# Kernel tuning notes

Measured on AMD Instinct MI355X. Metric: run time of the kernel, lower is better.

The kernel has to match this reference:

```python
import jax, jax.numpy as jnp
import numpy as np

EPS = 1e-5  # torch LayerNorm default
N_BLOCKS = 8
N_NODES = 4096
BATCH = 4096


def setup_inputs() -> dict:
    key = jax.random.key(0)
    ks = jax.random.split(key, 4)
    scale = 1.0 / np.sqrt(N_NODES)  # keep activations sane through 8 GEMMs
    x = jax.random.normal(ks[0], (BATCH, N_NODES), dtype=jnp.float32)
    W = jax.random.normal(ks[1], (N_BLOCKS, N_NODES, N_NODES), dtype=jnp.float32) * scale
    b = jax.random.normal(ks[2], (N_BLOCKS, N_NODES), dtype=jnp.float32) * 0.01
    slope = jax.random.uniform(ks[3], (N_BLOCKS, N_NODES), dtype=jnp.float32)
    ln_g = jnp.ones((N_BLOCKS, N_NODES), dtype=jnp.float32)
    ln_b = jnp.zeros((N_BLOCKS, N_NODES), dtype=jnp.float32)
    return {"x": x, "ln_g": ln_g, "ln_b": ln_b, "W": W, "b": b, "slope": slope}


def _block(x, g, bt, Wi, bi, si):
    # LayerNorm over last dim (biased variance, eps inside sqrt) -> Linear -> per-feature LeakyReLU
    mu = jnp.mean(x, axis=-1, keepdims=True)
    var = jnp.mean(jnp.square(x - mu), axis=-1, keepdims=True)
    ln = (x - mu) * jax.lax.rsqrt(var + EPS) * g + bt
    y = jnp.einsum('bn,mn->bm', ln, Wi) + bi  # torch Linear: x @ W.T + b
    return jnp.where(y < 0, y * si, y)


def reference(x, ln_g, ln_b, W, b, slope):
    for i in range(N_BLOCKS):
        x = _block(x, ln_g[i], ln_b[i], W[i], b[i], slope[i])
    return x
```

## Files before the change

### kernel.cpp

```cpp
#include <hip/hip_runtime.h>
#include <hip/hip_bf16.h>

#define NNODES 4096
#define NBATCH 4096
#define NBLK 8
#define LN_EPS 1e-5f

typedef __attribute__((ext_vector_type(8))) short short8;
typedef __attribute__((ext_vector_type(4))) float f32x4;
typedef __attribute__((ext_vector_type(4))) unsigned short u16x4;
typedef unsigned short u16;

__device__ __forceinline__ u16 bf16_rn(float f) {
  unsigned int u = __builtin_bit_cast(unsigned int, f);
  u += 0x7fffu + ((u >> 16) & 1u);
  return (u16)(u >> 16);
}

__device__ __forceinline__ float bf16_to_f(u16 h) {
  unsigned int u = ((unsigned int)h) << 16;
  return __builtin_bit_cast(float, u);
}

__device__ __forceinline__ void load_lds16(const void* g, void* l) {
  __builtin_amdgcn_global_load_lds((const __attribute__((address_space(1))) void*)g,
                                   (__attribute__((address_space(3))) void*)l,
                                   16, 0, 0);
}

template <bool LNF32>
__global__ __launch_bounds__(256) void prep_kernel(const float* __restrict__ W,
                                                   u16* __restrict__ Wb,
                                                   const void* __restrict__ xin,
                                                   const float* __restrict__ g,
                                                   const float* __restrict__ bt,
                                                   u16* __restrict__ lnout) {
  __shared__ float sh[8];
  int t = threadIdx.x;
  if (blockIdx.x < 16384) {
    int idx = blockIdx.x * 256 + t;
    float4 v = ((const float4*)W)[idx];
    u16x4 o;
    o[0] = bf16_rn(v.x); o[1] = bf16_rn(v.y); o[2] = bf16_rn(v.z); o[3] = bf16_rn(v.w);
    ((u16x4*)Wb)[idx] = o;
    return;
  }
  int row = blockIdx.x - 16384;
  float f[16];
  float s = 0.f, ss = 0.f;
  const float4* xr = (const float4*)((const float*)xin + (size_t)row * NNODES);
#pragma unroll
  for (int q = 0; q < 4; ++q) {
    float4 v = xr[q * 256 + t];
    f[q * 4 + 0] = v.x; f[q * 4 + 1] = v.y; f[q * 4 + 2] = v.z; f[q * 4 + 3] = v.w;
    s  += v.x + v.y + v.z + v.w;
    ss += v.x * v.x + v.y * v.y + v.z * v.z + v.w * v.w;
  }
#pragma unroll
  for (int off = 32; off >= 1; off >>= 1) {
    s  += __shfl_xor(s, off, 64);
    ss += __shfl_xor(ss, off, 64);
  }
  int wid = t >> 6, lane = t & 63;
  if (lane == 0) { sh[wid] = s; sh[wid + 4] = ss; }
  __syncthreads();
  s  = sh[0] + sh[1] + sh[2] + sh[3];
  ss = sh[4] + sh[5] + sh[6] + sh[7];
  float mu  = s * (1.f / NNODES);
  float var = ss * (1.f / NNODES) - mu * mu;
  float rs  = rsqrtf(var + LN_EPS);
  u16x4* o = (u16x4*)(lnout + (size_t)row * NNODES);
  const float4* gv = (const float4*)g;
  const float4* bv = (const float4*)bt;
#pragma unroll
  for (int q = 0; q < 4; ++q) {
    int i = q * 256 + t;
    float4 gg = gv[i], bb = bv[i];
    u16x4 ov;
    ov[0] = bf16_rn((f[q * 4 + 0] - mu) * rs * gg.x + bb.x);
    ov[1] = bf16_rn((f[q * 4 + 1] - mu) * rs * gg.y + bb.y);
    ov[2] = bf16_rn((f[q * 4 + 2] - mu) * rs * gg.z + bb.z);
    ov[3] = bf16_rn((f[q * 4 + 3] - mu) * rs * gg.w + bb.w);
    o[i] = ov;
  }
}

__global__ __launch_bounds__(256) void ln_bf16_kernel(const u16* __restrict__ x,
                                                      const float* __restrict__ g,
                                                      const float* __restrict__ bt,
                                                      u16* __restrict__ out) {
  int row = blockIdx.x;
  int t = threadIdx.x;
  const u16* xr = x + (size_t)row * NNODES;
  float f[2][8];
  float s = 0.f, ss = 0.f;
#pragma unroll
  for (int q = 0; q < 2; ++q) {
    short8 v = *(const short8*)(xr + q * 2048 + t * 8);
#pragma unroll
    for (int j = 0; j < 8; ++j) {
      float fv = bf16_to_f((u16)v[j]);
      f[q][j] = fv;
      s += fv; ss += fv * fv;
    }
  }
#pragma unroll
  for (int off = 32; off >= 1; off >>= 1) {
    s  += __shfl_xor(s, off, 64);
    ss += __shfl_xor(ss, off, 64);
  }
  __shared__ float sh[8];
  int wid = t >> 6, lane = t & 63;
  if (lane == 0) { sh[wid] = s; sh[wid + 4] = ss; }
  __syncthreads();
  s  = sh[0] + sh[1] + sh[2] + sh[3];
  ss = sh[4] + sh[5] + sh[6] + sh[7];
  float mu  = s * (1.f / NNODES);
  float var = ss * (1.f / NNODES) - mu * mu;
  float rs  = rsqrtf(var + LN_EPS);
  const float4* gv = (const float4*)g;
  const float4* bv = (const float4*)bt;
#pragma unroll
  for (int q = 0; q < 2; ++q) {
    int base = q * 2048 + t * 8;
    float4 g0 = gv[base / 4], g1 = gv[base / 4 + 1];
    float4 b0 = bv[base / 4], b1 = bv[base / 4 + 1];
    short8 sv;
    sv[0] = (short)bf16_rn((f[q][0] - mu) * rs * g0.x + b0.x);
    sv[1] = (short)bf16_rn((f[q][1] - mu) * rs * g0.y + b0.y);
    sv[2] = (short)bf16_rn((f[q][2] - mu) * rs * g0.z + b0.z);
    sv[3] = (short)bf16_rn((f[q][3] - mu) * rs * g0.w + b0.w);
    sv[4] = (short)bf16_rn((f[q][4] - mu) * rs * g1.x + b1.x);
    sv[5] = (short)bf16_rn((f[q][5] - mu) * rs * g1.y + b1.y);
    sv[6] = (short)bf16_rn((f[q][6] - mu) * rs * g1.z + b1.z);
    sv[7] = (short)bf16_rn((f[q][7] - mu) * rs * g1.w + b1.w);
    *(short8*)(out + (size_t)row * NNODES + base) = sv;
  }
}


#define VMC(N) asm volatile("s_waitcnt vmcnt(" #N ")" ::: "memory")

#define STAGE_A(T, H)                                                          \
  { load_lds16(Asrc0 + (size_t)((H) * 128) * Kdim + (T) * 64,                  \
               ldsA + ((T) & 1) * 16384 + (H) * 8192 + tid * 8);               \
    load_lds16(Asrc0 + (size_t)((H) * 128 + 64) * Kdim + (T) * 64,             \
               ldsA + ((T) & 1) * 16384 + (H) * 8192 + 4096 + tid * 8); }

#define STAGE_B(T, H)                                                          \
  { load_lds16(Bsrc0 + (size_t)((H) * 128) * Kdim + (T) * 64,                  \
               ldsB + ((T) & 1) * 16384 + (H) * 8192 + tid * 8);               \
    load_lds16(Bsrc0 + (size_t)((H) * 128 + 64) * Kdim + (T) * 64,             \
               ldsB + ((T) & 1) * 16384 + (H) * 8192 + 4096 + tid * 8); }

#define CVSTORE(SRC, CIDX)                                                     \
  { __builtin_amdgcn_sched_barrier(0);                                         \
    u16x4 o_;                                                                  \
    o_[0] = bf16_rn(SRC[0]); o_[1] = bf16_rn(SRC[1]);                          \
    o_[2] = bf16_rn(SRC[2]); o_[3] = bf16_rn(SRC[3]);                          \
    *(u16x4*)(Wnd + cvoff + (size_t)(CIDX) * 2048) = o_; }

#define CONVP3                                                                 \
  { if (CONVON && t < 16) {                                                    \
      const float* cp_ = Wns + cvoff + (size_t)(2 * t) * 2048;                 \
      asm volatile("global_load_dwordx4 %0, %1, off"                           \
                   : "=&v"(cvA) : "v"(cp_) : "memory");                        \
    }                                                                          \
    VMC(4);                                                                    \
    if (CONVON && t >= 1 && t <= 16) CVSTORE(cvB, 2 * t - 1) }

#define CONVP7                                                                 \
  { if (CONVON && t < 16) {                                                    \
      const float* cp_ = Wns + cvoff + (size_t)(2 * t + 1) * 2048;             \
      asm volatile("global_load_dwordx4 %0, %1, off"                           \
                   : "=&v"(cvB) : "v"(cp_) : "memory");                        \
    }                                                                          \
    VMC(4);                                                                    \
    if (CONVON && t < 16) CVSTORE(cvA, 2 * t) }

#define PH(KT, MH, NH, STAGE_STMT, VM_STMT)                                    \
  {                                                                            \
    const u16* Ab = ldsA + ((KT) & 1) * 16384 + aBase + (MH) * 4096;           \
    const u16* Bb = ldsB + ((KT) & 1) * 16384 + bBase + (NH) * 2048;           \
    if ((NH) == 0) {                                                           \
      _Pragma("unroll") for (int mi = 0; mi < 4; ++mi) {                       \
        afr[mi][0] = *(const short8*)(Ab + mi * 1024 + gk0);                   \
        afr[mi][1] = *(const short8*)(Ab + mi * 1024 + gk1);                   \
      }                                                                        \
    }                                                                          \
    if ((MH) == 0) {                                                           \
      _Pragma("unroll") for (int ni = 0; ni < 2; ++ni) {                       \
        bfr[NH][ni][0] = *(const short8*)(Bb + ni * 1024 + gk0);               \
        bfr[NH][ni][1] = *(const short8*)(Bb + ni * 1024 + gk1);               \
      }                                                                        \
    }                                                                          \
    STAGE_STMT;                                                                \
    if ((NH) == 0 && (MH) == 0)                                                \
      asm volatile("s_waitcnt lgkmcnt(8)" ::: "memory");                       \
    VM_STMT;                                                                   \
    __builtin_amdgcn_s_barrier();                                              \
    asm volatile("s_waitcnt lgkmcnt(0)" ::: "memory");                         \
    __builtin_amdgcn_sched_barrier(0);                                         \
    __builtin_amdgcn_s_setprio(1);                                             \
    _Pragma("unroll") for (int mi = 0; mi < 4; ++mi)                           \
      _Pragma("unroll") for (int ni = 0; ni < 2; ++ni) {                       \
        acc[(MH) * 4 + mi][(NH) * 2 + ni] =                                    \
          __builtin_amdgcn_mfma_f32_16x16x32_bf16(afr[mi][0], bfr[NH][ni][0],  \
            acc[(MH) * 4 + mi][(NH) * 2 + ni], 0, 0, 0);                       \
        acc[(MH) * 4 + mi][(NH) * 2 + ni] =                                    \
          __builtin_amdgcn_mfma_f32_16x16x32_bf16(afr[mi][1], bfr[NH][ni][1],  \
            acc[(MH) * 4 + mi][(NH) * 2 + ni], 0, 0, 0);                       \
      }                                                                        \
    __builtin_amdgcn_s_setprio(0);                                             \
    __builtin_amdgcn_s_barrier();                                              \
  }

template <bool OUTF32, bool CONVON>
__global__ __launch_bounds__(512, 2) void gemm256_kernel(const u16* __restrict__ A,
                                                         const u16* __restrict__ B,
                                                         const float* __restrict__ bias,
                                                         const float* __restrict__ slope,
                                                         void* __restrict__ Cv,
                                                         const float* __restrict__ Wns,
                                                         u16* __restrict__ Wnd) {
  constexpr int Kdim = NNODES;
  __shared__ u16 lds[65536];
  u16* ldsA = lds;
  u16* ldsB = lds + 32768;

  const int tid  = threadIdx.x;
  const int lane = tid & 63;
  const int wid  = tid >> 6;
  const int wr   = wid >> 2;
  const int wc   = wid & 3;

  int bid = blockIdx.x;
  int swz = (bid & 7) * 32 + (bid >> 3);
  const int brow = (swz >> 4) * 256;
  const int bcol = (swz & 15) * 256;

  const int srow = tid >> 3;
  const int sg   = ((tid & 7) ^ (srow & 7)) * 8;
  const u16* Asrc0 = A + (size_t)(brow + srow) * Kdim + sg;
  const u16* Bsrc0 = B + (size_t)(bcol + srow) * Kdim + sg;

  const int r16 = lane & 15, kq = lane >> 4;
  const int g0  = kq ^ (r16 & 7);
  const int gk0 = g0 * 8, gk1 = (g0 ^ 4) * 8;
  const int aBase = wr * 8192 + r16 * 64;
  const int bBase = (wc >> 1) * 8192 + ((wc & 1) * 64 + r16) * 64;

  const size_t cvoff = (size_t)bid * 65536 + tid * 4;
  f32x4 cvA, cvB;

  f32x4 acc[8][4] = {};
  short8 afr[4][2], bfr[2][2][2];

  STAGE_B(0, 0) STAGE_B(0, 1) STAGE_A(0, 0) STAGE_A(0, 1) STAGE_B(1, 0) STAGE_B(1, 1)
  VMC(4);
  __builtin_amdgcn_s_barrier();

  for (int t = 0; t < 31; ++t) {
    const int T = 2 * t;
    PH(T,     0, 0, STAGE_A(T + 1, 0), ;)
    PH(T,     0, 1, STAGE_A(T + 1, 1), ;)
    PH(T,     1, 0, STAGE_B(T + 2, 0), ;)
    PH(T,     1, 1, STAGE_B(T + 2, 1), CONVP3)
    PH(T + 1, 0, 0, STAGE_A(T + 2, 0), ;)
    PH(T + 1, 0, 1, STAGE_A(T + 2, 1), ;)
    PH(T + 1, 1, 0, STAGE_B(T + 3, 0), ;)
    PH(T + 1, 1, 1, STAGE_B(T + 3, 1), CONVP7)
  }
  PH(62, 0, 0, STAGE_A(63, 0), ;)
  PH(62, 0, 1, STAGE_A(63, 1), ;)
  PH(62, 1, 0, ;, ;)
  PH(62, 1, 1, ;, VMC(0))
  PH(63, 0, 0, ;, ;)
  PH(63, 0, 1, ;, ;)
  PH(63, 1, 0, ;, ;)
  PH(63, 1, 1, ;, ;)

  const int crow0 = brow + wr * 128 + (lane >> 4) * 4;
  const int ccol0 = bcol + wc * 64 + r16;
#pragma unroll
  for (int n = 0; n < 4; ++n) {
    int col = ccol0 + n * 16;
    float bv = bias[col], sv = slope[col];
#pragma unroll
    for (int m = 0; m < 8; ++m) {
      int row0 = crow0 + m * 16;
#pragma unroll
      for (int r = 0; r < 4; ++r) {
        float vv = acc[m][n][r] + bv;
        vv = vv < 0.f ? vv * sv : vv;
        if constexpr (OUTF32) {
          ((float*)Cv)[(size_t)(row0 + r) * NNODES + col] = vv;
        } else {
          ((u16*)Cv)[(size_t)(row0 + r) * NNODES + col] = bf16_rn(vv);
        }
      }
    }
  }
}

extern "C" void kernel_launch(void* const* d_in, const int* in_sizes, int n_in,
                              void* d_out, int out_size, void* d_ws, size_t ws_size,
                              hipStream_t stream) {
  const float* x     = (const float*)d_in[0];
  const float* ln_g  = (const float*)d_in[1];
  const float* ln_b  = (const float*)d_in[2];
  const float* W     = (const float*)d_in[3];
  const float* b     = (const float*)d_in[4];
  const float* slope = (const float*)d_in[5];
  float* out = (float*)d_out;

  char* ws = (char*)d_ws;
  u16* Wbuf0 = (u16*)ws;
  u16* Wbuf1 = (u16*)(ws + (size_t)32 * 1024 * 1024);
  u16* lnbuf = (u16*)(ws + (size_t)64 * 1024 * 1024);
  u16* ybuf  = (u16*)(ws + (size_t)96 * 1024 * 1024);

  const size_t WN = (size_t)NNODES * NNODES;

  for (int i = 0; i < NBLK; ++i) {
    u16* Wc = (i & 1) ? Wbuf1 : Wbuf0;
    u16* Wn = (i & 1) ? Wbuf0 : Wbuf1;
    if (i == 0)
      prep_kernel<true><<<dim3(16384 + NBATCH), dim3(256), 0, stream>>>(
          W, Wbuf0, (const void*)x, ln_g, ln_b, lnbuf);
    else
      ln_bf16_kernel<<<dim3(NBATCH), dim3(256), 0, stream>>>(
          ybuf, ln_g + (size_t)i * NNODES, ln_b + (size_t)i * NNODES, lnbuf);

    if (i == NBLK - 1)
      gemm256_kernel<true, false><<<dim3(256), dim3(512), 0, stream>>>(
          lnbuf, Wc, b + (size_t)i * NNODES, slope + (size_t)i * NNODES,
          (void*)out, nullptr, nullptr);
    else
      gemm256_kernel<false, true><<<dim3(256), dim3(512), 0, stream>>>(
          lnbuf, Wc, b + (size_t)i * NNODES, slope + (size_t)i * NNODES,
          (void*)ybuf, W + WN * (i + 1), Wn);
  }
}
```

Measured before the change: 1.095 ms.

## Drop trailing per-phase barrier and reschedule GEMM staging and weight conversion

```diff
diff --git a/kernel.cpp b/kernel.cpp
--- a/kernel.cpp
+++ b/kernel.cpp
@@ -28,10 +28,9 @@
                                    16, 0, 0);
 }
 
-template <bool LNF32>
 __global__ __launch_bounds__(256) void prep_kernel(const float* __restrict__ W,
                                                    u16* __restrict__ Wb,
-                                                   const void* __restrict__ xin,
+                                                   const float* __restrict__ xin,
                                                    const float* __restrict__ g,
                                                    const float* __restrict__ bt,
                                                    u16* __restrict__ lnout) {
@@ -48,7 +47,7 @@
   int row = blockIdx.x - 16384;
   float f[16];
   float s = 0.f, ss = 0.f;
-  const float4* xr = (const float4*)((const float*)xin + (size_t)row * NNODES);
+  const float4* xr = (const float4*)(xin + (size_t)row * NNODES);
 #pragma unroll
   for (int q = 0; q < 4; ++q) {
     float4 v = xr[q * 256 + t];
@@ -154,31 +153,34 @@
                ldsB + ((T) & 1) * 16384 + (H) * 8192 + 4096 + tid * 8); }
 
 #define CVSTORE(SRC, CIDX)                                                     \
-  { __builtin_amdgcn_sched_barrier(0);                                         \
-    u16x4 o_;                                                                  \
+  { u16x4 o_;                                                                  \
     o_[0] = bf16_rn(SRC[0]); o_[1] = bf16_rn(SRC[1]);                          \
     o_[2] = bf16_rn(SRC[2]); o_[3] = bf16_rn(SRC[3]);                          \
     *(u16x4*)(Wnd + cvoff + (size_t)(CIDX) * 2048) = o_; }
 
-#define CONVP3                                                                 \
-  { if (CONVON && t < 16) {                                                    \
-      const float* cp_ = Wns + cvoff + (size_t)(2 * t) * 2048;                 \
-      asm volatile("global_load_dwordx4 %0, %1, off"                           \
-                   : "=&v"(cvA) : "v"(cp_) : "memory");                        \
+#define CONVP2                                                                 \
+  { if (CONVON && t >= 1 && t <= 16) {                                         \
+      __builtin_amdgcn_sched_barrier(0);                                       \
+      CVSTORE(cvA, 2 * (t - 1))                                                \
+      CVSTORE(cvB, 2 * (t - 1) + 1)                                            \
     }                                                                          \
-    VMC(4);                                                                    \
-    if (CONVON && t >= 1 && t <= 16) CVSTORE(cvB, 2 * t - 1) }
-
-#define CONVP7                                                                 \
-  { if (CONVON && t < 16) {                                                    \
-      const float* cp_ = Wns + cvoff + (size_t)(2 * t + 1) * 2048;             \
-      asm volatile("global_load_dwordx4 %0, %1, off"                           \
-                   : "=&v"(cvB) : "v"(cp_) : "memory");                        \
-    }                                                                          \
-    VMC(4);                                                                    \
-    if (CONVON && t < 16) CVSTORE(cvA, 2 * t) }
-
-#define PH(KT, MH, NH, STAGE_STMT, VM_STMT)                                    \
+    if (CONVON && t < 16) {                                                    \
+      const float* cpa_ = Wns + cvoff + (size_t)(2 * t) * 2048;                \
+      const float* cpb_ = Wns + cvoff + (size_t)(2 * t + 1) * 2048;            \
+      asm volatile("global_load_dwordx4 %0, %2, off\n\t"                       \
+                   "global_load_dwordx4 %1, %3, off"                           \
+                   : "=&v"(cvA), "=&v"(cvB) : "v"(cpa_), "v"(cpb_)             \
+                   : "memory");                                                \
+    } }
+
+#define VMP3                                                                   \
+  { if (CONVON) {                                                              \
+      if (t == 0 || t == 16) { VMC(4); }                                       \
+      else if (t < 16)       { VMC(6); }                                       \
+      else                   { VMC(2); }                                       \
+    } else { VMC(2); } }
+
+#define PH1(KT, MH, NH, STAGE_STMT, VM_STMT)                                   \
   {                                                                            \
     const u16* Ab = ldsA + ((KT) & 1) * 16384 + aBase + (MH) * 4096;           \
     const u16* Bb = ldsB + ((KT) & 1) * 16384 + bBase + (NH) * 2048;           \
@@ -212,7 +214,6 @@
             acc[(MH) * 4 + mi][(NH) * 2 + ni], 0, 0, 0);                       \
       }                                                                        \
     __builtin_amdgcn_s_setprio(0);                                             \
-    __builtin_amdgcn_s_barrier();                                              \
   }
 
 template <bool OUTF32, bool CONVON>
@@ -262,23 +263,23 @@
 
   for (int t = 0; t < 31; ++t) {
     const int T = 2 * t;
-    PH(T,     0, 0, STAGE_A(T + 1, 0), ;)
-    PH(T,     0, 1, STAGE_A(T + 1, 1), ;)
-    PH(T,     1, 0, STAGE_B(T + 2, 0), ;)
-    PH(T,     1, 1, STAGE_B(T + 2, 1), CONVP3)
-    PH(T + 1, 0, 0, STAGE_A(T + 2, 0), ;)
-    PH(T + 1, 0, 1, STAGE_A(T + 2, 1), ;)
-    PH(T + 1, 1, 0, STAGE_B(T + 3, 0), ;)
-    PH(T + 1, 1, 1, STAGE_B(T + 3, 1), CONVP7)
-  }
-  PH(62, 0, 0, STAGE_A(63, 0), ;)
-  PH(62, 0, 1, STAGE_A(63, 1), ;)
-  PH(62, 1, 0, ;, ;)
-  PH(62, 1, 1, ;, VMC(0))
-  PH(63, 0, 0, ;, ;)
-  PH(63, 0, 1, ;, ;)
-  PH(63, 1, 0, ;, ;)
-  PH(63, 1, 1, ;, ;)
+    PH1(T,     0, 0, STAGE_A(T + 1, 0), ;)
+    PH1(T,     0, 1, STAGE_A(T + 1, 1), ;)
+    PH1(T,     1, 0, CONVP2,            ;)
+    PH1(T,     1, 1, STAGE_B(T + 2, 0), VMP3)
+    PH1(T + 1, 0, 0, STAGE_B(T + 2, 1), ;)
+    PH1(T + 1, 0, 1, STAGE_A(T + 2, 0), ;)
+    PH1(T + 1, 1, 0, STAGE_A(T + 2, 1), ;)
+    PH1(T + 1, 1, 1, { STAGE_B(T + 3, 0) STAGE_B(T + 3, 1) }, VMC(4))
+  }
+  PH1(62, 0, 0, STAGE_A(63, 0), ;)
+  PH1(62, 0, 1, STAGE_A(63, 1), ;)
+  PH1(62, 1, 0, ;, ;)
+  PH1(62, 1, 1, ;, VMC(0))
+  PH1(63, 0, 0, ;, ;)
+  PH1(63, 0, 1, ;, ;)
+  PH1(63, 1, 0, ;, ;)
+  PH1(63, 1, 1, ;, ;)
 
   const int crow0 = brow + wr * 128 + (lane >> 4) * 4;
   const int ccol0 = bcol + wc * 64 + r16;
@@ -326,8 +327,8 @@
     u16* Wc = (i & 1) ? Wbuf1 : Wbuf0;
     u16* Wn = (i & 1) ? Wbuf0 : Wbuf1;
     if (i == 0)
-      prep_kernel<true><<<dim3(16384 + NBATCH), dim3(256), 0, stream>>>(
-          W, Wbuf0, (const void*)x, ln_g, ln_b, lnbuf);
+      prep_kernel<<<dim3(16384 + NBATCH), dim3(256), 0, stream>>>(
+          W, Wbuf0, x, ln_g, ln_b, lnbuf);
     else
       ln_bf16_kernel<<<dim3(NBATCH), dim3(256), 0, stream>>>(
           ybuf, ln_g + (size_t)i * NNODES, ln_b + (size_t)i * NNODES, lnbuf);
```

Result: faster. 1.049 ms (median of 4 runs) (-4.2%).
